# Kernel optimization log

Measured on AMD Instinct MI355X. Metric: run time of the kernel, lower is better.

The kernel has to match this reference:

```python
import jax, jax.numpy as jnp
import numpy as np

B, N1, N2 = 4, 2048, 1024
IN_DIM, OUT_DIM, H = 768, 1024, 16
DH = OUT_DIM // H  # 64
EPS = 1e-5


def _layernorm(x, g, b):
    mu = jnp.mean(x, axis=-1, keepdims=True)
    var = jnp.var(x, axis=-1, keepdims=True)
    return (x - mu) * jax.lax.rsqrt(var + EPS) * g + b


def setup_inputs() -> dict:
    key = jax.random.key(0)
    ks = jax.random.split(key, 16)
    s_in = 1.0 / np.sqrt(IN_DIM)
    s_out = 1.0 / np.sqrt(OUT_DIM)
    return {
        "input": jax.random.normal(ks[0], (B, N1, IN_DIM), jnp.float32),
        "output": jax.random.normal(ks[1], (B, N2, OUT_DIM), jnp.float32),
        "q_w": jax.random.uniform(ks[2], (OUT_DIM, OUT_DIM), jnp.float32, -s_out, s_out),
        "q_b": jax.random.uniform(ks[3], (OUT_DIM,), jnp.float32, -s_out, s_out),
        "k_w": jax.random.uniform(ks[4], (OUT_DIM, IN_DIM), jnp.float32, -s_in, s_in),
        "k_b": jax.random.uniform(ks[5], (OUT_DIM,), jnp.float32, -s_in, s_in),
        "v_w": jax.random.uniform(ks[6], (OUT_DIM, IN_DIM), jnp.float32, -s_in, s_in),
        "v_b": jax.random.uniform(ks[7], (OUT_DIM,), jnp.float32, -s_in, s_in),
        "proj_w": jax.random.uniform(ks[8], (OUT_DIM, OUT_DIM), jnp.float32, -s_out, s_out),
        "proj_b": jax.random.uniform(ks[9], (OUT_DIM,), jnp.float32, -s_out, s_out),
        "ln_in_g": jnp.ones((IN_DIM,), jnp.float32),
        "ln_in_b": jnp.zeros((IN_DIM,), jnp.float32),
        "ln_out_g": jnp.ones((OUT_DIM,), jnp.float32),
        "ln_out_b": jnp.zeros((OUT_DIM,), jnp.float32),
    }


def reference(input, output, q_w, q_b, k_w, k_b, v_w, v_b, proj_w, proj_b,
              ln_in_g, ln_in_b, ln_out_g, ln_out_b):
    i = _layernorm(input, ln_in_g, ln_in_b)            # [B,N1,IN]
    o = _layernorm(output, ln_out_g, ln_out_b)         # [B,N2,OUT]
    q = (o @ q_w.T + q_b).reshape(B, N2, H, DH)        # [B,N2,H,DH]
    k = (i @ k_w.T + k_b).reshape(B, N1, H, DH)
    v = (i @ v_w.T + v_b).reshape(B, N1, H, DH)
    scores = jnp.einsum("bqhd,bkhd->bhqk", q, k) / np.sqrt(DH).astype(np.float32)
    att_probs = jax.nn.softmax(scores, axis=-1)        # [B,H,N2,N1]
    ctrl = jnp.einsum("bhqk,bkhd->bqhd", att_probs, v).reshape(B, N2, OUT_DIM)
    out = output + (ctrl @ proj_w.T + proj_b)          # residual (DropPath p=0 is identity)
    return (att_probs, out)
```

## Files before the change

### kernel.cpp

```cpp
#include <hip/hip_runtime.h>
#include <hip/hip_bf16.h>
#include <math.h>


typedef __attribute__((ext_vector_type(8))) short short8;
typedef __attribute__((ext_vector_type(4))) float f32x4;

__device__ __forceinline__ ushort f2b(float f) {
  __hip_bfloat16 h = __float2bfloat16(f);
  return *reinterpret_cast<ushort*>(&h);
}

__device__ __forceinline__ void gload16(const ushort* g, ushort* lds) {
  __builtin_amdgcn_global_load_lds(
      (const __attribute__((address_space(1))) unsigned int*)g,
      (__attribute__((address_space(3))) unsigned int*)lds, 16, 0, 0);
}

__device__ __forceinline__ float wave_red_sum(float v) {
#pragma unroll
  for (int o = 32; o; o >>= 1) v += __shfl_down(v, o);
  return v;
}

__device__ __forceinline__ void ln_row(const float* __restrict__ x,
                                       const float* __restrict__ g,
                                       const float* __restrict__ bta,
                                       ushort* __restrict__ y, int D) {
  int nv = D >> 2;
  float s = 0.f, s2 = 0.f;
  for (int i = threadIdx.x; i < nv; i += 256) {
    float4 v = ((const float4*)x)[i];
    s += v.x + v.y + v.z + v.w;
    s2 += v.x * v.x + v.y * v.y + v.z * v.z + v.w * v.w;
  }
  s = wave_red_sum(s);
  s2 = wave_red_sum(s2);
  __shared__ float red[8];
  int wid = threadIdx.x >> 6, lane = threadIdx.x & 63;
  if (lane == 0) { red[wid] = s; red[4 + wid] = s2; }
  __syncthreads();
  float ts = red[0] + red[1] + red[2] + red[3];
  float t2 = red[4] + red[5] + red[6] + red[7];
  float mu = ts / (float)D;
  float rstd = rsqrtf(t2 / (float)D - mu * mu + 1e-5f);
  for (int i = threadIdx.x; i < nv; i += 256) {
    float4 v = ((const float4*)x)[i];
    float4 gg = ((const float4*)g)[i];
    float4 bb = ((const float4*)bta)[i];
    ushort4 o;
    o.x = f2b((v.x - mu) * rstd * gg.x + bb.x);
    o.y = f2b((v.y - mu) * rstd * gg.y + bb.y);
    o.z = f2b((v.z - mu) * rstd * gg.z + bb.z);
    o.w = f2b((v.w - mu) * rstd * gg.w + bb.w);
    ((ushort4*)y)[i] = o;
  }
}

__global__ __launch_bounds__(256) void prep_kernel(
    const float* __restrict__ s0, ushort* __restrict__ d0,
    const float* __restrict__ s1, ushort* __restrict__ d1,
    const float* __restrict__ s2, ushort* __restrict__ d2,
    const float* __restrict__ s3, ushort* __restrict__ d3,
    const float* __restrict__ inA, const float* __restrict__ gA,
    const float* __restrict__ bA, ushort* __restrict__ yA,
    const float* __restrict__ inB, const float* __restrict__ gB,
    const float* __restrict__ bB, ushort* __restrict__ yB) {
  int blk = blockIdx.x;
  if (blk < 3584) {
    int i = blk * 256 + threadIdx.x;
    const float* s;
    ushort* d;
    int j = i;
    if (i < 262144) { s = s0; d = d0; }
    else if (i < 458752) { s = s1; d = d1; j = i - 262144; }
    else if (i < 655360) { s = s2; d = d2; j = i - 458752; }
    else { s = s3; d = d3; j = i - 655360; }
    float4 v = ((const float4*)s)[j];
    ushort4 o;
    o.x = f2b(v.x); o.y = f2b(v.y); o.z = f2b(v.z); o.w = f2b(v.w);
    ((ushort4*)d)[j] = o;
  } else {
    size_t r = blk - 3584;
    if (r < 8192)
      ln_row(inA + r * 768, gA, bA, yA + r * 768, 768);
    else {
      size_t rr = r - 8192;
      ln_row(inB + rr * 1024, gB, bB, yB + rr * 1024, 1024);
    }
  }
}

__global__ __launch_bounds__(256) void qkv_kernel(
    const ushort* __restrict__ o_ln, const ushort* __restrict__ i_ln,
    const ushort* __restrict__ qwb, const ushort* __restrict__ kwb,
    const ushort* __restrict__ vwb, const float* __restrict__ q_b,
    const float* __restrict__ k_b, const float* __restrict__ v_b,
    ushort* __restrict__ qb, ushort* __restrict__ kb,
    ushort* __restrict__ vt) {
  __shared__ __align__(16) ushort As[3][128 * 32];
  __shared__ __align__(16) ushort Ws[3][64 * 32];

  int id = blockIdx.x;
  const ushort *A, *W;
  const float* bias;
  ushort* C;
  int K, lda, ldw, ldc, bx, by, biasmode;
  long long coff = 0;
  if (id < 512) {
    A = o_ln; W = qwb; bias = q_b; C = qb;
    K = 1024; lda = 1024; ldw = 1024; ldc = 1024;
    bx = id & 31; by = id >> 5; biasmode = 1;
  } else if (id < 1536) {
    int t = id - 512;
    A = i_ln; W = kwb; bias = k_b; C = kb;
    K = 768; lda = 768; ldw = 768; ldc = 1024;
    bx = t & 63; by = t >> 6; biasmode = 1;
  } else {
    int t = id - 1536;
    int z = t >> 8, r = t & 255;
    A = vwb; W = i_ln + (size_t)z * 1572864; bias = v_b; C = vt;
    coff = (long long)z * 2097152;
    K = 768; lda = 768; ldw = 768; ldc = 2048;
    bx = r & 7; by = r >> 3; biasmode = 2;
  }

  const ushort* Ab = A + (size_t)bx * 128 * lda;
  const ushort* Wb = W + (size_t)by * 64 * ldw;
  int tid = threadIdx.x, l = tid & 63, w = tid >> 6;
  int wr = w >> 1, wc = w & 1;
  f32x4 acc[4][2];
#pragma unroll
  for (int i = 0; i < 4; ++i)
#pragma unroll
    for (int j = 0; j < 2; ++j) acc[i][j] = (f32x4){0.f, 0.f, 0.f, 0.f};

  int srow = l >> 2, scol = (l & 3) * 8;
  int lr = l & 15, lk = (l >> 4) * 8;

#define STAGE(bb, k0)                                                       \
  do {                                                                      \
    const ushort* ga = Ab + (size_t)(w * 32 + srow) * lda + (k0) + scol;    \
    gload16(ga, &As[bb][(w * 32) * 32]);                                    \
    gload16(ga + (size_t)16 * lda, &As[bb][(w * 32 + 16) * 32]);            \
    gload16(Wb + (size_t)(w * 16 + srow) * ldw + (k0) + scol,               \
            &Ws[bb][(w * 16) * 32]);                                        \
  } while (0)

  int nk = K >> 5;
  STAGE(0, 0);
  STAGE(1, 32);
  int cur = 0;
  for (int t = 0; t < nk; ++t) {
    if (t + 2 < nk) {
      int slot = cur + 2;
      if (slot >= 3) slot -= 3;
      STAGE(slot, (t + 2) * 32);
      asm volatile("s_waitcnt vmcnt(6)" ::: "memory");
    } else if (t + 1 < nk) {
      asm volatile("s_waitcnt vmcnt(3)" ::: "memory");
    } else {
      asm volatile("s_waitcnt vmcnt(0)" ::: "memory");
    }
    __builtin_amdgcn_s_barrier();
    __builtin_amdgcn_sched_barrier(0);
    short8 af[4], bf[2];
#pragma unroll
    for (int fi = 0; fi < 4; ++fi)
      af[fi] = *(const short8*)&As[cur][(wr * 64 + fi * 16 + lr) * 32 + lk];
#pragma unroll
    for (int fj = 0; fj < 2; ++fj)
      bf[fj] = *(const short8*)&Ws[cur][(wc * 32 + fj * 16 + lr) * 32 + lk];
    __builtin_amdgcn_s_setprio(1);
#pragma unroll
    for (int fi = 0; fi < 4; ++fi)
#pragma unroll
      for (int fj = 0; fj < 2; ++fj)
        acc[fi][fj] = __builtin_amdgcn_mfma_f32_16x16x32_bf16(
            af[fi], bf[fj], acc[fi][fj], 0, 0, 0);
    __builtin_amdgcn_s_setprio(0);
    __builtin_amdgcn_s_barrier();
    cur = cur + 1;
    if (cur >= 3) cur -= 3;
  }
#undef STAGE

  int m0 = bx * 128, n0 = by * 64;
#pragma unroll
  for (int fi = 0; fi < 4; ++fi)
#pragma unroll
    for (int fj = 0; fj < 2; ++fj) {
      int col = n0 + wc * 32 + fj * 16 + lr;
      float bv = (biasmode == 1) ? bias[col] : 0.f;
#pragma unroll
      for (int r4 = 0; r4 < 4; ++r4) {
        int row = m0 + wr * 64 + fi * 16 + (l >> 4) * 4 + r4;
        float val = acc[fi][fj][r4] + bv;
        if (biasmode == 2) val += bias[row];
        C[coff + (size_t)row * ldc + col] = f2b(val);
      }
    }
}

__global__ __launch_bounds__(256) void proj_kernel(
    const ushort* __restrict__ A, const ushort* __restrict__ W,
    const float* __restrict__ bias, const float* __restrict__ resid,
    float* __restrict__ C) {
  __shared__ __align__(16) ushort As[3][128 * 32];
  __shared__ __align__(16) ushort Ws[3][64 * 32];
  const int lda = 1024, ldw = 1024, ldc = 1024, nk = 32;
  const ushort* Ab = A + (size_t)blockIdx.x * 128 * lda;
  const ushort* Wb = W + (size_t)blockIdx.y * 64 * ldw;
  int tid = threadIdx.x, l = tid & 63, w = tid >> 6;
  int wr = w >> 1, wc = w & 1;
  f32x4 acc[4][2];
#pragma unroll
  for (int i = 0; i < 4; ++i)
#pragma unroll
    for (int j = 0; j < 2; ++j) acc[i][j] = (f32x4){0.f, 0.f, 0.f, 0.f};

  int srow = l >> 2, scol = (l & 3) * 8;
  int lr = l & 15, lk = (l >> 4) * 8;

#define STAGE(bb, k0)                                                       \
  do {                                                                      \
    const ushort* ga = Ab + (size_t)(w * 32 + srow) * lda + (k0) + scol;    \
    gload16(ga, &As[bb][(w * 32) * 32]);                                    \
    gload16(ga + (size_t)16 * lda, &As[bb][(w * 32 + 16) * 32]);            \
    gload16(Wb + (size_t)(w * 16 + srow) * ldw + (k0) + scol,               \
            &Ws[bb][(w * 16) * 32]);                                        \
  } while (0)

  STAGE(0, 0);
  STAGE(1, 32);
  int cur = 0;
  for (int t = 0; t < nk; ++t) {
    if (t + 2 < nk) {
      int slot = cur + 2;
      if (slot >= 3) slot -= 3;
      STAGE(slot, (t + 2) * 32);
      asm volatile("s_waitcnt vmcnt(6)" ::: "memory");
    } else if (t + 1 < nk) {
      asm volatile("s_waitcnt vmcnt(3)" ::: "memory");
    } else {
      asm volatile("s_waitcnt vmcnt(0)" ::: "memory");
    }
    __builtin_amdgcn_s_barrier();
    __builtin_amdgcn_sched_barrier(0);
    short8 af[4], bf[2];
#pragma unroll
    for (int fi = 0; fi < 4; ++fi)
      af[fi] = *(const short8*)&As[cur][(wr * 64 + fi * 16 + lr) * 32 + lk];
#pragma unroll
    for (int fj = 0; fj < 2; ++fj)
      bf[fj] = *(const short8*)&Ws[cur][(wc * 32 + fj * 16 + lr) * 32 + lk];
    __builtin_amdgcn_s_setprio(1);
#pragma unroll
    for (int fi = 0; fi < 4; ++fi)
#pragma unroll
      for (int fj = 0; fj < 2; ++fj)
        acc[fi][fj] = __builtin_amdgcn_mfma_f32_16x16x32_bf16(
            af[fi], bf[fj], acc[fi][fj], 0, 0, 0);
    __builtin_amdgcn_s_setprio(0);
    __builtin_amdgcn_s_barrier();
    cur = cur + 1;
    if (cur >= 3) cur -= 3;
  }
#undef STAGE

  int m0 = blockIdx.x * 128, n0 = blockIdx.y * 64;
#pragma unroll
  for (int fi = 0; fi < 4; ++fi)
#pragma unroll
    for (int fj = 0; fj < 2; ++fj) {
      int col = n0 + wc * 32 + fj * 16 + lr;
      float bv = bias[col];
#pragma unroll
      for (int r4 = 0; r4 < 4; ++r4) {
        int row = m0 + wr * 64 + fi * 16 + (l >> 4) * 4 + r4;
        C[(size_t)row * ldc + col] =
            acc[fi][fj][r4] + bv + resid[(size_t)row * ldc + col];
      }
    }
}

__global__ __launch_bounds__(256, 3) void attn_kernel(
    const ushort* __restrict__ qb, const ushort* __restrict__ kb,
    const ushort* __restrict__ vt, float* __restrict__ att,
    ushort* __restrict__ ctrl) {
  __shared__ ushort QP_lds[64 * 72];
  __shared__ ushort K_lds[2][64 * 72];
  __shared__ ushort V_lds[2][64 * 72];

  int bid = blockIdx.x;
  int vv = ((bid & 7) << 7) + (bid >> 3);
  int bh = vv >> 4, mt = vv & 15;
  int b = bh >> 4, h = bh & 15;
  int m0 = mt * 64;
  int tid = threadIdx.x, l = tid & 63, w = tid >> 6;
  int lr = l & 15, lk = (l >> 4) * 8;
  int klo = (l >> 4) * 4;

  const float SC = 0.125f * 1.44269504088896f;

#pragma unroll
  for (int it = 0; it < 2; ++it) {
    int idx = tid + it * 256;
    int row = idx >> 3, c8 = (idx & 7) * 8;
    *(uint4*)&QP_lds[row * 72 + c8] = *(const uint4*)(
        qb + (size_t)(b * 1024 + m0 + row) * 1024 + h * 64 + c8);
  }
  __syncthreads();
  short8 aq0 = *(const short8*)&QP_lds[(w * 16 + lr) * 72 + lk];
  short8 aq1 = *(const short8*)&QP_lds[(w * 16 + lr) * 72 + 32 + lk];
  __syncthreads();

  const size_t kbase = (size_t)b * 2048 * 1024 + h * 64;
  const ushort* Kb = kb + kbase;
  int srow = tid >> 3, sc8 = (tid & 7) * 8;

  float ls = 0.f;

  uint4 kr0 = *(const uint4*)(Kb + (size_t)srow * 1024 + sc8);
  uint4 kr1 = *(const uint4*)(Kb + (size_t)(srow + 32) * 1024 + sc8);
  for (int t = 0; t < 32; ++t) {
    int cur = t & 1;
    *(uint4*)&K_lds[cur][srow * 72 + sc8] = kr0;
    *(uint4*)&K_lds[cur][(srow + 32) * 72 + sc8] = kr1;
    asm volatile("s_waitcnt lgkmcnt(0)" ::: "memory");
    __builtin_amdgcn_s_barrier();
    __builtin_amdgcn_sched_barrier(0);
    if (t < 31) {
      kr0 = *(const uint4*)(Kb + (size_t)(t * 64 + 64 + srow) * 1024 + sc8);
      kr1 = *(const uint4*)(Kb + (size_t)(t * 64 + 96 + srow) * 1024 + sc8);
    }
    f32x4 acc[4];
    __builtin_amdgcn_s_setprio(1);
#pragma unroll
    for (int fj = 0; fj < 4; ++fj) {
      short8 kf0 = *(const short8*)&K_lds[cur][(fj * 16 + lr) * 72 + lk];
      short8 kf1 = *(const short8*)&K_lds[cur][(fj * 16 + lr) * 72 + 32 + lk];
      f32x4 a = (f32x4){0.f, 0.f, 0.f, 0.f};
      a = __builtin_amdgcn_mfma_f32_16x16x32_bf16(kf0, aq0, a, 0, 0, 0);
      a = __builtin_amdgcn_mfma_f32_16x16x32_bf16(kf1, aq1, a, 0, 0, 0);
      acc[fj] = a;
    }
    __builtin_amdgcn_s_setprio(0);
#pragma unroll
    for (int fj = 0; fj < 4; ++fj)
#pragma unroll
      for (int r = 0; r < 4; ++r) ls += exp2f(acc[fj][r] * SC);
  }
  ls += __shfl_xor(ls, 16);
  ls += __shfl_xor(ls, 32);
  float mb = __log2f(ls);

  float* attp = att + (size_t)bh * 2048 * 1024 + (size_t)m0 * 2048;
  const ushort* Vb = vt + (size_t)bh * 64 * 2048;
  int qrow = w * 16 + lr;
  f32x4 acco[4];
#pragma unroll
  for (int fd = 0; fd < 4; ++fd) acco[fd] = (f32x4){0.f, 0.f, 0.f, 0.f};

  kr0 = *(const uint4*)(Kb + (size_t)srow * 1024 + sc8);
  kr1 = *(const uint4*)(Kb + (size_t)(srow + 32) * 1024 + sc8);
  uint4 vr0 = *(const uint4*)(Vb + (size_t)srow * 2048 + sc8);
  uint4 vr1 = *(const uint4*)(Vb + (size_t)(srow + 32) * 2048 + sc8);
  for (int t = 0; t < 32; ++t) {
    int cur = t & 1;
    int k0 = t * 64;
    *(uint4*)&K_lds[cur][srow * 72 + sc8] = kr0;
    *(uint4*)&K_lds[cur][(srow + 32) * 72 + sc8] = kr1;
    *(uint4*)&V_lds[cur][srow * 72 + sc8] = vr0;
    *(uint4*)&V_lds[cur][(srow + 32) * 72 + sc8] = vr1;
    asm volatile("s_waitcnt lgkmcnt(0)" ::: "memory");
    __builtin_amdgcn_s_barrier();
    __builtin_amdgcn_sched_barrier(0);
    if (t < 31) {
      kr0 = *(const uint4*)(Kb + (size_t)(k0 + 64 + srow) * 1024 + sc8);
      kr1 = *(const uint4*)(Kb + (size_t)(k0 + 96 + srow) * 1024 + sc8);
      vr0 = *(const uint4*)(Vb + (size_t)srow * 2048 + k0 + 64 + sc8);
      vr1 = *(const uint4*)(Vb + (size_t)(srow + 32) * 2048 + k0 + 64 + sc8);
    }
    f32x4 acc[4];
    __builtin_amdgcn_s_setprio(1);
#pragma unroll
    for (int fj = 0; fj < 4; ++fj) {
      short8 kf0 = *(const short8*)&K_lds[cur][(fj * 16 + lr) * 72 + lk];
      short8 kf1 = *(const short8*)&K_lds[cur][(fj * 16 + lr) * 72 + 32 + lk];
      f32x4 a = (f32x4){0.f, 0.f, 0.f, 0.f};
      a = __builtin_amdgcn_mfma_f32_16x16x32_bf16(kf0, aq0, a, 0, 0, 0);
      a = __builtin_amdgcn_mfma_f32_16x16x32_bf16(kf1, aq1, a, 0, 0, 0);
      acc[fj] = a;
    }
    __builtin_amdgcn_s_setprio(0);
#pragma unroll
    for (int fj = 0; fj < 4; ++fj) {
      f32x4 p;
      p[0] = exp2f(fmaf(acc[fj][0], SC, -mb));
      p[1] = exp2f(fmaf(acc[fj][1], SC, -mb));
      p[2] = exp2f(fmaf(acc[fj][2], SC, -mb));
      p[3] = exp2f(fmaf(acc[fj][3], SC, -mb));
      __builtin_nontemporal_store(
          p, (f32x4*)(attp + (size_t)qrow * 2048 + k0 + fj * 16 + klo));
      union { uint2 u; ushort s[4]; } pk;
      pk.s[0] = f2b(p[0]);
      pk.s[1] = f2b(p[1]);
      pk.s[2] = f2b(p[2]);
      pk.s[3] = f2b(p[3]);
      *(uint2*)&QP_lds[qrow * 72 + fj * 16 + klo] = pk.u;
    }
    short8 ap0 = *(const short8*)&QP_lds[(w * 16 + lr) * 72 + lk];
    short8 ap1 = *(const short8*)&QP_lds[(w * 16 + lr) * 72 + 32 + lk];
    __builtin_amdgcn_s_setprio(1);
#pragma unroll
    for (int fd = 0; fd < 4; ++fd) {
      short8 bv0 = *(const short8*)&V_lds[cur][(fd * 16 + lr) * 72 + lk];
      short8 bv1 = *(const short8*)&V_lds[cur][(fd * 16 + lr) * 72 + 32 + lk];
      acco[fd] =
          __builtin_amdgcn_mfma_f32_16x16x32_bf16(ap0, bv0, acco[fd], 0, 0, 0);
      acco[fd] =
          __builtin_amdgcn_mfma_f32_16x16x32_bf16(ap1, bv1, acco[fd], 0, 0, 0);
    }
    __builtin_amdgcn_s_setprio(0);
  }

#pragma unroll
  for (int fd = 0; fd < 4; ++fd)
#pragma unroll
    for (int r = 0; r < 4; ++r) {
      int wrow = w * 16 + (l >> 4) * 4 + r;
      ctrl[(size_t)(b * 1024 + m0 + wrow) * 1024 + h * 64 + fd * 16 + lr] =
          f2b(acco[fd][r]);
    }
}

extern "C" void kernel_launch(void* const* d_in, const int* in_sizes, int n_in,
                              void* d_out, int out_size, void* d_ws,
                              size_t ws_size, hipStream_t stream) {
  const float* input = (const float*)d_in[0];
  const float* output = (const float*)d_in[1];
  const float* q_w = (const float*)d_in[2];
  const float* q_b = (const float*)d_in[3];
  const float* k_w = (const float*)d_in[4];
  const float* k_b = (const float*)d_in[5];
  const float* v_w = (const float*)d_in[6];
  const float* v_b = (const float*)d_in[7];
  const float* p_w = (const float*)d_in[8];
  const float* p_b = (const float*)d_in[9];
  const float* ln_in_g = (const float*)d_in[10];
  const float* ln_in_b = (const float*)d_in[11];
  const float* ln_out_g = (const float*)d_in[12];
  const float* ln_out_b = (const float*)d_in[13];

  ushort* ws = (ushort*)d_ws;
  ushort* i_ln = ws;
  ushort* o_ln = i_ln + 6291456;
  ushort* qb = o_ln + 4194304;
  ushort* kb = qb + 4194304;
  ushort* vt = kb + 8388608;
  ushort* ctrl = vt + 8388608;
  ushort* qwb = ctrl + 4194304;
  ushort* kwb = qwb + 1048576;
  ushort* vwb = kwb + 786432;
  ushort* pwb = vwb + 786432;

  float* att = (float*)d_out;
  float* out2 = att + 134217728LL;

  prep_kernel<<<15872, 256, 0, stream>>>(q_w, qwb, k_w, kwb, v_w, vwb, p_w,
                                         pwb, input, ln_in_g, ln_in_b, i_ln,
                                         output, ln_out_g, ln_out_b, o_ln);

  qkv_kernel<<<2560, 256, 0, stream>>>(o_ln, i_ln, qwb, kwb, vwb, q_b, k_b,
                                       v_b, qb, kb, vt);

  attn_kernel<<<dim3(1024), 256, 0, stream>>>(qb, kb, vt, att, ctrl);

  proj_kernel<<<dim3(32, 16), 256, 0, stream>>>(ctrl, pwb, p_b, output, out2);
}
```

Measured before the change: 281.1 us.

## Enlarge QKV GEMM tiles to 128x128 and process 128 query rows per attention block

The QKV GEMM now uses 128x128 output tiles with double buffering instead of 128x64 tiles with triple buffering, halving the grid and reusing each A fragment across four B fragments. The attention kernel handles 128 query rows per block (two 64-row fragments per wave), so each K/V tile loaded into LDS is reused across twice as many queries and the grid is halved. The aim is to cut redundant global K/V and weight loads per FLOP. The cost is more registers and LDS per block, lower occupancy (launch bounds reduced to 2) and fewer blocks on a 256-CU part, which may leave units idle.

```diff
diff --git a/kernel.cpp b/kernel.cpp
--- a/kernel.cpp
+++ b/kernel.cpp
@@ -98,35 +98,113 @@
     const float* __restrict__ k_b, const float* __restrict__ v_b,
     ushort* __restrict__ qb, ushort* __restrict__ kb,
     ushort* __restrict__ vt) {
-  __shared__ __align__(16) ushort As[3][128 * 32];
-  __shared__ __align__(16) ushort Ws[3][64 * 32];
+  __shared__ __align__(16) ushort As[2][128 * 32];
+  __shared__ __align__(16) ushort Ws[2][128 * 32];
 
   int id = blockIdx.x;
   const ushort *A, *W;
   const float* bias;
   ushort* C;
-  int K, lda, ldw, ldc, bx, by, biasmode;
+  int K, lda, ldc, bx, by, biasmode;
   long long coff = 0;
-  if (id < 512) {
+  if (id < 256) {
     A = o_ln; W = qwb; bias = q_b; C = qb;
-    K = 1024; lda = 1024; ldw = 1024; ldc = 1024;
+    K = 1024; lda = 1024; ldc = 1024;
     bx = id & 31; by = id >> 5; biasmode = 1;
-  } else if (id < 1536) {
-    int t = id - 512;
+  } else if (id < 768) {
+    int t = id - 256;
     A = i_ln; W = kwb; bias = k_b; C = kb;
-    K = 768; lda = 768; ldw = 768; ldc = 1024;
+    K = 768; lda = 768; ldc = 1024;
     bx = t & 63; by = t >> 6; biasmode = 1;
   } else {
-    int t = id - 1536;
-    int z = t >> 8, r = t & 255;
+    int t = id - 768;
+    int z = t >> 7, r = t & 127;
     A = vwb; W = i_ln + (size_t)z * 1572864; bias = v_b; C = vt;
     coff = (long long)z * 2097152;
-    K = 768; lda = 768; ldw = 768; ldc = 2048;
+    K = 768; lda = 768; ldc = 2048;
     bx = r & 7; by = r >> 3; biasmode = 2;
   }
 
   const ushort* Ab = A + (size_t)bx * 128 * lda;
-  const ushort* Wb = W + (size_t)by * 64 * ldw;
+  const ushort* Wb = W + (size_t)by * 128 * lda;
+  int tid = threadIdx.x, l = tid & 63, w = tid >> 6;
+  int wr = w >> 1, wc = w & 1;
+  f32x4 acc[4][4];
+#pragma unroll
+  for (int i = 0; i < 4; ++i)
+#pragma unroll
+    for (int j = 0; j < 4; ++j) acc[i][j] = (f32x4){0.f, 0.f, 0.f, 0.f};
+
+  int srow = l >> 2, scol = (l & 3) * 8;
+  int lr = l & 15, lk = (l >> 4) * 8;
+
+#define STAGE(bb, k0)                                                       \
+  do {                                                                      \
+    const ushort* ga = Ab + (size_t)(w * 16 + srow) * lda + (k0) + scol;    \
+    const ushort* gw = Wb + (size_t)(w * 16 + srow) * lda + (k0) + scol;    \
+    gload16(ga, &As[bb][(w * 16) * 32]);                                    \
+    gload16(ga + (size_t)64 * lda, &As[bb][(w * 16 + 64) * 32]);            \
+    gload16(gw, &Ws[bb][(w * 16) * 32]);                                    \
+    gload16(gw + (size_t)64 * lda, &Ws[bb][(w * 16 + 64) * 32]);            \
+  } while (0)
+
+  int nk = K >> 5;
+  STAGE(0, 0);
+  for (int t = 0; t < nk; ++t) {
+    int cur = t & 1;
+    if (t + 1 < nk) {
+      STAGE(cur ^ 1, (t + 1) * 32);
+      asm volatile("s_waitcnt vmcnt(4)" ::: "memory");
+    } else {
+      asm volatile("s_waitcnt vmcnt(0)" ::: "memory");
+    }
+    __builtin_amdgcn_s_barrier();
+    __builtin_amdgcn_sched_barrier(0);
+    short8 af[4], bf[4];
+#pragma unroll
+    for (int fi = 0; fi < 4; ++fi)
+      af[fi] = *(const short8*)&As[cur][(wr * 64 + fi * 16 + lr) * 32 + lk];
+#pragma unroll
+    for (int fj = 0; fj < 4; ++fj)
+      bf[fj] = *(const short8*)&Ws[cur][(wc * 64 + fj * 16 + lr) * 32 + lk];
+    __builtin_amdgcn_s_setprio(1);
+#pragma unroll
+    for (int fi = 0; fi < 4; ++fi)
+#pragma unroll
+      for (int fj = 0; fj < 4; ++fj)
+        acc[fi][fj] = __builtin_amdgcn_mfma_f32_16x16x32_bf16(
+            af[fi], bf[fj], acc[fi][fj], 0, 0, 0);
+    __builtin_amdgcn_s_setprio(0);
+    __builtin_amdgcn_s_barrier();
+  }
+#undef STAGE
+
+  int m0 = bx * 128, n0 = by * 128;
+#pragma unroll
+  for (int fi = 0; fi < 4; ++fi)
+#pragma unroll
+    for (int fj = 0; fj < 4; ++fj) {
+      int col = n0 + wc * 64 + fj * 16 + lr;
+      float bv = (biasmode == 1) ? bias[col] : 0.f;
+#pragma unroll
+      for (int r4 = 0; r4 < 4; ++r4) {
+        int row = m0 + wr * 64 + fi * 16 + (l >> 4) * 4 + r4;
+        float val = acc[fi][fj][r4] + bv;
+        if (biasmode == 2) val += bias[row];
+        C[coff + (size_t)row * ldc + col] = f2b(val);
+      }
+    }
+}
+
+__global__ __launch_bounds__(256) void proj_kernel(
+    const ushort* __restrict__ A, const ushort* __restrict__ W,
+    const float* __restrict__ bias, const float* __restrict__ resid,
+    float* __restrict__ C) {
+  __shared__ __align__(16) ushort As[3][128 * 32];
+  __shared__ __align__(16) ushort Ws[3][64 * 32];
+  const int lda = 1024, ldw = 1024, ldc = 1024, nk = 32;
+  const ushort* Ab = A + (size_t)blockIdx.x * 128 * lda;
+  const ushort* Wb = W + (size_t)blockIdx.y * 64 * ldw;
   int tid = threadIdx.x, l = tid & 63, w = tid >> 6;
   int wr = w >> 1, wc = w & 1;
   f32x4 acc[4][2];
@@ -147,7 +225,6 @@
             &Ws[bb][(w * 16) * 32]);                                        \
   } while (0)
 
-  int nk = K >> 5;
   STAGE(0, 0);
   STAGE(1, 32);
   int cur = 0;
@@ -185,89 +262,6 @@
   }
 #undef STAGE
 
-  int m0 = bx * 128, n0 = by * 64;
-#pragma unroll
-  for (int fi = 0; fi < 4; ++fi)
-#pragma unroll
-    for (int fj = 0; fj < 2; ++fj) {
-      int col = n0 + wc * 32 + fj * 16 + lr;
-      float bv = (biasmode == 1) ? bias[col] : 0.f;
-#pragma unroll
-      for (int r4 = 0; r4 < 4; ++r4) {
-        int row = m0 + wr * 64 + fi * 16 + (l >> 4) * 4 + r4;
-        float val = acc[fi][fj][r4] + bv;
-        if (biasmode == 2) val += bias[row];
-        C[coff + (size_t)row * ldc + col] = f2b(val);
-      }
-    }
-}
-
-__global__ __launch_bounds__(256) void proj_kernel(
-    const ushort* __restrict__ A, const ushort* __restrict__ W,
-    const float* __restrict__ bias, const float* __restrict__ resid,
-    float* __restrict__ C) {
-  __shared__ __align__(16) ushort As[3][128 * 32];
-  __shared__ __align__(16) ushort Ws[3][64 * 32];
-  const int lda = 1024, ldw = 1024, ldc = 1024, nk = 32;
-  const ushort* Ab = A + (size_t)blockIdx.x * 128 * lda;
-  const ushort* Wb = W + (size_t)blockIdx.y * 64 * ldw;
-  int tid = threadIdx.x, l = tid & 63, w = tid >> 6;
-  int wr = w >> 1, wc = w & 1;
-  f32x4 acc[4][2];
-#pragma unroll
-  for (int i = 0; i < 4; ++i)
-#pragma unroll
-    for (int j = 0; j < 2; ++j) acc[i][j] = (f32x4){0.f, 0.f, 0.f, 0.f};
-
-  int srow = l >> 2, scol = (l & 3) * 8;
-  int lr = l & 15, lk = (l >> 4) * 8;
-
-#define STAGE(bb, k0)                                                       \
-  do {                                                                      \
-    const ushort* ga = Ab + (size_t)(w * 32 + srow) * lda + (k0) + scol;    \
-    gload16(ga, &As[bb][(w * 32) * 32]);                                    \
-    gload16(ga + (size_t)16 * lda, &As[bb][(w * 32 + 16) * 32]);            \
-    gload16(Wb + (size_t)(w * 16 + srow) * ldw + (k0) + scol,               \
-            &Ws[bb][(w * 16) * 32]);                                        \
-  } while (0)
-
-  STAGE(0, 0);
-  STAGE(1, 32);
-  int cur = 0;
-  for (int t = 0; t < nk; ++t) {
-    if (t + 2 < nk) {
-      int slot = cur + 2;
-      if (slot >= 3) slot -= 3;
-      STAGE(slot, (t + 2) * 32);
-      asm volatile("s_waitcnt vmcnt(6)" ::: "memory");
-    } else if (t + 1 < nk) {
-      asm volatile("s_waitcnt vmcnt(3)" ::: "memory");
-    } else {
-      asm volatile("s_waitcnt vmcnt(0)" ::: "memory");
-    }
-    __builtin_amdgcn_s_barrier();
-    __builtin_amdgcn_sched_barrier(0);
-    short8 af[4], bf[2];
-#pragma unroll
-    for (int fi = 0; fi < 4; ++fi)
-      af[fi] = *(const short8*)&As[cur][(wr * 64 + fi * 16 + lr) * 32 + lk];
-#pragma unroll
-    for (int fj = 0; fj < 2; ++fj)
-      bf[fj] = *(const short8*)&Ws[cur][(wc * 32 + fj * 16 + lr) * 32 + lk];
-    __builtin_amdgcn_s_setprio(1);
-#pragma unroll
-    for (int fi = 0; fi < 4; ++fi)
-#pragma unroll
-      for (int fj = 0; fj < 2; ++fj)
-        acc[fi][fj] = __builtin_amdgcn_mfma_f32_16x16x32_bf16(
-            af[fi], bf[fj], acc[fi][fj], 0, 0, 0);
-    __builtin_amdgcn_s_setprio(0);
-    __builtin_amdgcn_s_barrier();
-    cur = cur + 1;
-    if (cur >= 3) cur -= 3;
-  }
-#undef STAGE
-
   int m0 = blockIdx.x * 128, n0 = blockIdx.y * 64;
 #pragma unroll
   for (int fi = 0; fi < 4; ++fi)
@@ -284,19 +278,19 @@
     }
 }
 
-__global__ __launch_bounds__(256, 3) void attn_kernel(
+__global__ __launch_bounds__(256, 2) void attn_kernel(
     const ushort* __restrict__ qb, const ushort* __restrict__ kb,
     const ushort* __restrict__ vt, float* __restrict__ att,
     ushort* __restrict__ ctrl) {
-  __shared__ ushort QP_lds[64 * 72];
+  __shared__ ushort QP_lds[128 * 72];
   __shared__ ushort K_lds[2][64 * 72];
   __shared__ ushort V_lds[2][64 * 72];
 
   int bid = blockIdx.x;
-  int vv = ((bid & 7) << 7) + (bid >> 3);
-  int bh = vv >> 4, mt = vv & 15;
+  int vv = ((bid & 7) << 6) + (bid >> 3);
+  int bh = vv >> 3, mt = vv & 7;
   int b = bh >> 4, h = bh & 15;
-  int m0 = mt * 64;
+  int m0 = mt * 128;
   int tid = threadIdx.x, l = tid & 63, w = tid >> 6;
   int lr = l & 15, lk = (l >> 4) * 8;
   int klo = (l >> 4) * 4;
@@ -304,22 +298,26 @@
   const float SC = 0.125f * 1.44269504088896f;
 
 #pragma unroll
-  for (int it = 0; it < 2; ++it) {
+  for (int it = 0; it < 4; ++it) {
     int idx = tid + it * 256;
     int row = idx >> 3, c8 = (idx & 7) * 8;
     *(uint4*)&QP_lds[row * 72 + c8] = *(const uint4*)(
         qb + (size_t)(b * 1024 + m0 + row) * 1024 + h * 64 + c8);
   }
   __syncthreads();
-  short8 aq0 = *(const short8*)&QP_lds[(w * 16 + lr) * 72 + lk];
-  short8 aq1 = *(const short8*)&QP_lds[(w * 16 + lr) * 72 + 32 + lk];
+  short8 aq[2][2];
+#pragma unroll
+  for (int f = 0; f < 2; ++f) {
+    aq[f][0] = *(const short8*)&QP_lds[(f * 64 + w * 16 + lr) * 72 + lk];
+    aq[f][1] = *(const short8*)&QP_lds[(f * 64 + w * 16 + lr) * 72 + 32 + lk];
+  }
   __syncthreads();
 
   const size_t kbase = (size_t)b * 2048 * 1024 + h * 64;
   const ushort* Kb = kb + kbase;
   int srow = tid >> 3, sc8 = (tid & 7) * 8;
 
-  float ls = 0.f;
+  float ls[2] = {0.f, 0.f};
 
   uint4 kr0 = *(const uint4*)(Kb + (size_t)srow * 1024 + sc8);
   uint4 kr1 = *(const uint4*)(Kb + (size_t)(srow + 32) * 1024 + sc8);
@@ -334,33 +332,43 @@
       kr0 = *(const uint4*)(Kb + (size_t)(t * 64 + 64 + srow) * 1024 + sc8);
       kr1 = *(const uint4*)(Kb + (size_t)(t * 64 + 96 + srow) * 1024 + sc8);
     }
-    f32x4 acc[4];
-    __builtin_amdgcn_s_setprio(1);
-#pragma unroll
-    for (int fj = 0; fj < 4; ++fj) {
-      short8 kf0 = *(const short8*)&K_lds[cur][(fj * 16 + lr) * 72 + lk];
-      short8 kf1 = *(const short8*)&K_lds[cur][(fj * 16 + lr) * 72 + 32 + lk];
-      f32x4 a = (f32x4){0.f, 0.f, 0.f, 0.f};
-      a = __builtin_amdgcn_mfma_f32_16x16x32_bf16(kf0, aq0, a, 0, 0, 0);
-      a = __builtin_amdgcn_mfma_f32_16x16x32_bf16(kf1, aq1, a, 0, 0, 0);
-      acc[fj] = a;
-    }
-    __builtin_amdgcn_s_setprio(0);
-#pragma unroll
-    for (int fj = 0; fj < 4; ++fj)
-#pragma unroll
-      for (int r = 0; r < 4; ++r) ls += exp2f(acc[fj][r] * SC);
-  }
-  ls += __shfl_xor(ls, 16);
-  ls += __shfl_xor(ls, 32);
-  float mb = __log2f(ls);
+#pragma unroll
+    for (int f = 0; f < 2; ++f) {
+      f32x4 acc[4];
+      __builtin_amdgcn_s_setprio(1);
+#pragma unroll
+      for (int fj = 0; fj < 4; ++fj) {
+        short8 kf0 = *(const short8*)&K_lds[cur][(fj * 16 + lr) * 72 + lk];
+        short8 kf1 =
+            *(const short8*)&K_lds[cur][(fj * 16 + lr) * 72 + 32 + lk];
+        f32x4 a = (f32x4){0.f, 0.f, 0.f, 0.f};
+        a = __builtin_amdgcn_mfma_f32_16x16x32_bf16(kf0, aq[f][0], a, 0, 0, 0);
+        a = __builtin_amdgcn_mfma_f32_16x16x32_bf16(kf1, aq[f][1], a, 0, 0, 0);
+        acc[fj] = a;
+      }
+      __builtin_amdgcn_s_setprio(0);
+#pragma unroll
+      for (int fj = 0; fj < 4; ++fj)
+#pragma unroll
+        for (int r = 0; r < 4; ++r) ls[f] += exp2f(acc[fj][r] * SC);
+    }
+  }
+  float mb[2];
+#pragma unroll
+  for (int f = 0; f < 2; ++f) {
+    float s = ls[f];
+    s += __shfl_xor(s, 16);
+    s += __shfl_xor(s, 32);
+    mb[f] = __log2f(s);
+  }
 
   float* attp = att + (size_t)bh * 2048 * 1024 + (size_t)m0 * 2048;
   const ushort* Vb = vt + (size_t)bh * 64 * 2048;
-  int qrow = w * 16 + lr;
-  f32x4 acco[4];
-#pragma unroll
-  for (int fd = 0; fd < 4; ++fd) acco[fd] = (f32x4){0.f, 0.f, 0.f, 0.f};
+  f32x4 acco[2][4];
+#pragma unroll
+  for (int f = 0; f < 2; ++f)
+#pragma unroll
+    for (int fd = 0; fd < 4; ++fd) acco[f][fd] = (f32x4){0.f, 0.f, 0.f, 0.f};
 
   kr0 = *(const uint4*)(Kb + (size_t)srow * 1024 + sc8);
   kr1 = *(const uint4*)(Kb + (size_t)(srow + 32) * 1024 + sc8);
@@ -382,57 +390,74 @@
       vr0 = *(const uint4*)(Vb + (size_t)srow * 2048 + k0 + 64 + sc8);
       vr1 = *(const uint4*)(Vb + (size_t)(srow + 32) * 2048 + k0 + 64 + sc8);
     }
-    f32x4 acc[4];
+    f32x4 acc[2][4];
     __builtin_amdgcn_s_setprio(1);
 #pragma unroll
     for (int fj = 0; fj < 4; ++fj) {
       short8 kf0 = *(const short8*)&K_lds[cur][(fj * 16 + lr) * 72 + lk];
       short8 kf1 = *(const short8*)&K_lds[cur][(fj * 16 + lr) * 72 + 32 + lk];
-      f32x4 a = (f32x4){0.f, 0.f, 0.f, 0.f};
-      a = __builtin_amdgcn_mfma_f32_16x16x32_bf16(kf0, aq0, a, 0, 0, 0);
-      a = __builtin_amdgcn_mfma_f32_16x16x32_bf16(kf1, aq1, a, 0, 0, 0);
-      acc[fj] = a;
+#pragma unroll
+      for (int f = 0; f < 2; ++f) {
+        f32x4 a = (f32x4){0.f, 0.f, 0.f, 0.f};
+        a = __builtin_amdgcn_mfma_f32_16x16x32_bf16(kf0, aq[f][0], a, 0, 0, 0);
+        a = __builtin_amdgcn_mfma_f32_16x16x32_bf16(kf1, aq[f][1], a, 0, 0, 0);
+        acc[f][fj] = a;
+      }
     }
     __builtin_amdgcn_s_setprio(0);
 #pragma unroll
-    for (int fj = 0; fj < 4; ++fj) {
-      f32x4 p;
-      p[0] = exp2f(fmaf(acc[fj][0], SC, -mb));
-      p[1] = exp2f(fmaf(acc[fj][1], SC, -mb));
-      p[2] = exp2f(fmaf(acc[fj][2], SC, -mb));
-      p[3] = exp2f(fmaf(acc[fj][3], SC, -mb));
-      __builtin_nontemporal_store(
-          p, (f32x4*)(attp + (size_t)qrow * 2048 + k0 + fj * 16 + klo));
-      union { uint2 u; ushort s[4]; } pk;
-      pk.s[0] = f2b(p[0]);
-      pk.s[1] = f2b(p[1]);
-      pk.s[2] = f2b(p[2]);
-      pk.s[3] = f2b(p[3]);
-      *(uint2*)&QP_lds[qrow * 72 + fj * 16 + klo] = pk.u;
-    }
-    short8 ap0 = *(const short8*)&QP_lds[(w * 16 + lr) * 72 + lk];
-    short8 ap1 = *(const short8*)&QP_lds[(w * 16 + lr) * 72 + 32 + lk];
+    for (int f = 0; f < 2; ++f) {
+      int qrow = f * 64 + w * 16 + lr;
+#pragma unroll
+      for (int fj = 0; fj < 4; ++fj) {
+        f32x4 p;
+        p[0] = exp2f(fmaf(acc[f][fj][0], SC, -mb[f]));
+        p[1] = exp2f(fmaf(acc[f][fj][1], SC, -mb[f]));
+        p[2] = exp2f(fmaf(acc[f][fj][2], SC, -mb[f]));
+        p[3] = exp2f(fmaf(acc[f][fj][3], SC, -mb[f]));
+        __builtin_nontemporal_store(
+            p, (f32x4*)(attp + (size_t)qrow * 2048 + k0 + fj * 16 + klo));
+        union { uint2 u; ushort s[4]; } pk;
+        pk.s[0] = f2b(p[0]);
+        pk.s[1] = f2b(p[1]);
+        pk.s[2] = f2b(p[2]);
+        pk.s[3] = f2b(p[3]);
+        *(uint2*)&QP_lds[qrow * 72 + fj * 16 + klo] = pk.u;
+      }
+    }
+    short8 ap[2][2];
+#pragma unroll
+    for (int f = 0; f < 2; ++f) {
+      ap[f][0] = *(const short8*)&QP_lds[(f * 64 + w * 16 + lr) * 72 + lk];
+      ap[f][1] =
+          *(const short8*)&QP_lds[(f * 64 + w * 16 + lr) * 72 + 32 + lk];
+    }
     __builtin_amdgcn_s_setprio(1);
 #pragma unroll
     for (int fd = 0; fd < 4; ++fd) {
       short8 bv0 = *(const short8*)&V_lds[cur][(fd * 16 + lr) * 72 + lk];
       short8 bv1 = *(const short8*)&V_lds[cur][(fd * 16 + lr) * 72 + 32 + lk];
-      acco[fd] =
-          __builtin_amdgcn_mfma_f32_16x16x32_bf16(ap0, bv0, acco[fd], 0, 0, 0);
-      acco[fd] =
-          __builtin_amdgcn_mfma_f32_16x16x32_bf16(ap1, bv1, acco[fd], 0, 0, 0);
+#pragma unroll
+      for (int f = 0; f < 2; ++f) {
+        acco[f][fd] = __builtin_amdgcn_mfma_f32_16x16x32_bf16(
+            ap[f][0], bv0, acco[f][fd], 0, 0, 0);
+        acco[f][fd] = __builtin_amdgcn_mfma_f32_16x16x32_bf16(
+            ap[f][1], bv1, acco[f][fd], 0, 0, 0);
+      }
     }
     __builtin_amdgcn_s_setprio(0);
   }
 
 #pragma unroll
-  for (int fd = 0; fd < 4; ++fd)
-#pragma unroll
-    for (int r = 0; r < 4; ++r) {
-      int wrow = w * 16 + (l >> 4) * 4 + r;
-      ctrl[(size_t)(b * 1024 + m0 + wrow) * 1024 + h * 64 + fd * 16 + lr] =
-          f2b(acco[fd][r]);
-    }
+  for (int f = 0; f < 2; ++f)
+#pragma unroll
+    for (int fd = 0; fd < 4; ++fd)
+#pragma unroll
+      for (int r = 0; r < 4; ++r) {
+        int wrow = f * 64 + w * 16 + (l >> 4) * 4 + r;
+        ctrl[(size_t)(b * 1024 + m0 + wrow) * 1024 + h * 64 + fd * 16 + lr] =
+            f2b(acco[f][fd][r]);
+      }
 }
 
 extern "C" void kernel_launch(void* const* d_in, const int* in_sizes, int n_in,
@@ -472,10 +497,10 @@
                                          pwb, input, ln_in_g, ln_in_b, i_ln,
                                          output, ln_out_g, ln_out_b, o_ln);
 
-  qkv_kernel<<<2560, 256, 0, stream>>>(o_ln, i_ln, qwb, kwb, vwb, q_b, k_b,
+  qkv_kernel<<<1280, 256, 0, stream>>>(o_ln, i_ln, qwb, kwb, vwb, q_b, k_b,
                                        v_b, qb, kb, vt);
 
-  attn_kernel<<<dim3(1024), 256, 0, stream>>>(qb, kb, vt, att, ctrl);
+  attn_kernel<<<dim3(512), 256, 0, stream>>>(qb, kb, vt, att, ctrl);
 
   proj_kernel<<<dim3(32, 16), 256, 0, stream>>>(ctrl, pwb, p_b, output, out2);
 }
```

Measured after the change: 320.4 us. +14.0%, slower.
